# Performance work log

Measured on AMD Instinct MI355X. Metric: run time of the kernel, lower is better.

## Reference

```python
import jax, jax.numpy as jnp
import numpy as np

N_NODES = 100000
N_EDGES = 1600000
IN_CH = 128
HID = 64
OUT_CH = 10
N_GRAPHS = 64
NEG_SLOPE = 0.2   # GATv2Conv default negative_slope
EPS = 1e-16       # PyG softmax eps


def setup_inputs() -> dict:
    key = jax.random.key(0)
    ks = jax.random.split(key, 10)
    x = jax.random.normal(ks[0], (N_NODES, IN_CH), dtype=jnp.float32)
    edge_index = jax.random.randint(ks[1], (2, N_EDGES), 0, N_NODES, dtype=jnp.int64)
    batch = jnp.sort(jax.random.randint(ks[2], (N_NODES,), 0, N_GRAPHS, dtype=jnp.int64))
    s = 1.0 / np.sqrt(IN_CH)
    Wl = jax.random.uniform(ks[3], (IN_CH, HID), jnp.float32, -s, s)   # lin_l (source)
    Wr = jax.random.uniform(ks[4], (IN_CH, HID), jnp.float32, -s, s)   # lin_r (target)
    att = jax.random.uniform(ks[5], (HID,), jnp.float32, -1.0 / np.sqrt(HID), 1.0 / np.sqrt(HID))
    bias = jnp.zeros((HID,), jnp.float32)
    sf = 1.0 / np.sqrt(HID)
    fc_w = jax.random.uniform(ks[6], (HID, OUT_CH), jnp.float32, -sf, sf)
    fc_b = jax.random.uniform(ks[7], (OUT_CH,), jnp.float32, -sf, sf)
    return {"x": x, "Wl": Wl, "Wr": Wr, "att": att, "bias": bias,
            "fc_w": fc_w, "fc_b": fc_b, "edge_index": edge_index, "batch": batch}


def reference(x, Wl, Wr, att, bias, fc_w, fc_b, edge_index, batch):
    src, tgt = edge_index[0], edge_index[1]
    # GATv2Conv, heads=1: separate linear for source/target
    xl = x @ Wl                         # [N, H] messages (source side)
    xr = x @ Wr                         # [N, H] target side
    z = xl[src] + xr[tgt]               # [E, H]
    e = jnp.where(z > 0, z, NEG_SLOPE * z) @ att   # [E]
    # segment softmax over incoming edges of each target node
    m = jax.ops.segment_max(e, tgt, num_segments=N_NODES)      # [N]
    a = jnp.exp(e - m[tgt])                                    # [E]
    denom = jax.ops.segment_sum(a, tgt, num_segments=N_NODES)  # [N]
    alpha = a / (denom[tgt] + EPS)                             # [E]
    out = jax.ops.segment_sum(alpha[:, None] * xl[src], tgt, num_segments=N_NODES)
    out = out + bias                                           # [N, H]
    # global mean pool over graphs
    cnt = jax.ops.segment_sum(jnp.ones((N_NODES,), out.dtype), batch, num_segments=N_GRAPHS)
    pooled = jax.ops.segment_sum(out, batch, num_segments=N_GRAPHS) / jnp.maximum(cnt, 1.0)[:, None]
    h = jnp.where(pooled > 0, pooled, 0.01 * pooled)           # F.leaky_relu default slope
    # dropout is identity in eval / p=0
    return h @ fc_w + fc_b                                     # [G, OUT_CH]
```

## Files before the change

### kernel.cpp

```cpp
#include <hip/hip_runtime.h>
#include <hip/hip_bf16.h>

#define NN 100000
#define EE 1600000
#define CIN 128
#define HID 64
#define NG 64
#define NOUT 10
#define BSZ 32
#define NB 3125
#define NBA 3136
#define CAP 768
#define NBC 196
#define CCAP 9216

typedef short s16x8 __attribute__((ext_vector_type(8)));
typedef float f32x4 __attribute__((ext_vector_type(4)));

__device__ __forceinline__ unsigned short f2b(float f) {
  unsigned int b = __float_as_uint(f);
  return (unsigned short)((b + 0x7FFFu + ((b >> 16) & 1u)) >> 16);
}
__device__ __forceinline__ float b2f_lo(unsigned int u) {
  return __uint_as_float(u << 16);
}
__device__ __forceinline__ float b2f_hi(unsigned int u) {
  return __uint_as_float(u & 0xFFFF0000u);
}

__global__ __launch_bounds__(256) void k_prep(const float* __restrict__ Wl,
                                              const float* __restrict__ Wr,
                                              unsigned short* __restrict__ Wt) {
  int flat = blockIdx.x * 2048 + threadIdx.x;
  for (int i = 0; i < 8; ++i, flat += 256) {
    int n = flat & 127, k = flat >> 7;
    float v = (n < 64) ? Wl[k * 64 + n] : Wr[k * 64 + (n - 64)];
    Wt[n * 128 + k] = f2b(v);
  }
}

__global__ __launch_bounds__(256) void k_gemm(
    const float* __restrict__ x, const unsigned short* __restrict__ Wt,
    unsigned short* __restrict__ xl, unsigned short* __restrict__ xr) {
  __shared__ unsigned short A[128 * 128];
  __shared__ unsigned short B[128 * 128];
  const int tid = threadIdx.x;
  const int lane = tid & 63;
  const int w = tid >> 6;
  const int nb = blockIdx.x * 128;

  {
    int u = tid;
#pragma unroll
    for (int i = 0; i < 8; ++i, u += 256) {
      int n = u >> 4, slot = u & 15;
      uint4 v = *(const uint4*)((const char*)Wt + u * 16);
      int addr = n * 256 + ((slot * 16) ^ ((n & 7) << 4));
      *(uint4*)((char*)B + addr) = v;
    }
  }
  {
    int f = tid;
#pragma unroll
    for (int i = 0; i < 16; ++i, f += 256) {
      int row = f >> 5, c4 = f & 31;
      int node = nb + row;
      float4 v = make_float4(0.f, 0.f, 0.f, 0.f);
      if (node < NN) v = *(const float4*)(x + (long)node * CIN + c4 * 4);
      uint2 p;
      p.x = (unsigned)f2b(v.x) | ((unsigned)f2b(v.y) << 16);
      p.y = (unsigned)f2b(v.z) | ((unsigned)f2b(v.w) << 16);
      int base16 = row * 256 + (((c4 >> 1) << 4) ^ ((row & 7) << 4));
      *(uint2*)((char*)A + base16 + (c4 & 1) * 8) = p;
    }
  }
  __syncthreads();

  const int m0 = w * 32;
  f32x4 acc[2][8];
#pragma unroll
  for (int mt = 0; mt < 2; ++mt)
#pragma unroll
    for (int nt = 0; nt < 8; ++nt) acc[mt][nt] = (f32x4){0.f, 0.f, 0.f, 0.f};

#pragma unroll
  for (int ks = 0; ks < 4; ++ks) {
    const int kb2 = (ks * 32 + (lane >> 4) * 8) * 2;
    const int r0 = m0 + (lane & 15);
    const int r1 = r0 + 16;
    s16x8 a0 = *(const s16x8*)((char*)A + r0 * 256 + (kb2 ^ ((r0 & 7) << 4)));
    s16x8 a1 = *(const s16x8*)((char*)A + r1 * 256 + (kb2 ^ ((r1 & 7) << 4)));
#pragma unroll
    for (int nt = 0; nt < 8; ++nt) {
      const int col = nt * 16 + (lane & 15);
      s16x8 b =
          *(const s16x8*)((char*)B + col * 256 + (kb2 ^ ((col & 7) << 4)));
      acc[0][nt] =
          __builtin_amdgcn_mfma_f32_16x16x32_bf16(a0, b, acc[0][nt], 0, 0, 0);
      acc[1][nt] =
          __builtin_amdgcn_mfma_f32_16x16x32_bf16(a1, b, acc[1][nt], 0, 0, 0);
    }
  }
  __syncthreads();

#pragma unroll
  for (int mt = 0; mt < 2; ++mt) {
    const int rowb = m0 + mt * 16 + (lane >> 4) * 4;
#pragma unroll
    for (int nt = 0; nt < 8; ++nt) {
      const int col = nt * 16 + (lane & 15);
#pragma unroll
      for (int r = 0; r < 4; ++r)
        *((unsigned short*)A + (rowb + r) * 128 + col) = f2b(acc[mt][nt][r]);
    }
  }
  __syncthreads();

  {
    int u = tid;
#pragma unroll
    for (int i = 0; i < 8; ++i, u += 256) {
      int row = u >> 4, slot = u & 15;
      int node = nb + row;
      if (node < NN) {
        uint4 v = *(const uint4*)((const char*)A + row * 256 + slot * 16);
        if (slot < 8)
          *(uint4*)((char*)xl + (long)node * 128 + slot * 16) = v;
        else
          *(uint4*)((char*)xr + (long)node * 128 + (slot - 8) * 16) = v;
      }
    }
  }
}

__global__ __launch_bounds__(256) void k_coarse(const int* __restrict__ ei,
                                                int* __restrict__ gcurc,
                                                unsigned int* __restrict__ coarse) {
  __shared__ int hist[NBC], lbase[NBC], cur[NBC];
  const int tid = threadIdx.x;
  const int base = blockIdx.x * 4096;
  int ss[16], tt[16];
  for (int b = tid; b < NBC; b += 256) hist[b] = 0;
#pragma unroll
  for (int i = 0; i < 16; ++i) {
    int j = base + i * 256 + tid;
    if (j < EE) {
      ss[i] = ei[j];
      tt[i] = ei[EE + j];
    } else {
      tt[i] = -1;
    }
  }
  __syncthreads();
#pragma unroll
  for (int i = 0; i < 16; ++i)
    if (tt[i] >= 0) atomicAdd(&hist[tt[i] >> 9], 1);
  __syncthreads();
  for (int b = tid; b < NBC; b += 256) {
    int c = hist[b];
    lbase[b] = c ? atomicAdd(gcurc + b, c) : 0;
    cur[b] = 0;
  }
  __syncthreads();
#pragma unroll
  for (int i = 0; i < 16; ++i) {
    if (tt[i] >= 0) {
      int cb = tt[i] >> 9;
      int p = lbase[cb] + atomicAdd(&cur[cb], 1);
      if (p < CCAP)
        coarse[(long)cb * CCAP + p] =
            ((unsigned)ss[i] << 9) | (unsigned)(tt[i] & 511);
    }
  }
}

__global__ __launch_bounds__(256) void k_fine(
    const int* __restrict__ gcurc, const unsigned int* __restrict__ coarse,
    unsigned int* __restrict__ buckets, unsigned short* __restrict__ sc16,
    int* __restrict__ gcnt) {
  __shared__ unsigned int staged[CCAP];
  __shared__ int hist[512], sc[512], cur[512];
  __shared__ int ex32[16], csum[4], coffs[4];
  const int tid = threadIdx.x;
  const int c = blockIdx.x;
  const int ecnt = min(gcurc[c], CCAP);

  for (int i = tid; i < 512; i += 256) hist[i] = 0;
  __syncthreads();
  for (int i = tid; i < ecnt; i += 256) {
    unsigned v = coarse[(long)c * CCAP + i];
    staged[i] = v;
    atomicAdd(&hist[v & 511u], 1);
  }
  __syncthreads();

  {
    const int w = tid >> 6, lane = tid & 63;
    const int iA = w * 128 + lane, iB = iA + 64;
    int sA = hist[iA], sB = hist[iB];
#pragma unroll
    for (int off = 1; off < 64; off <<= 1) {
      int t1 = __shfl_up(sA, off, 64);
      int t2 = __shfl_up(sB, off, 64);
      if (lane >= off) { sA += t1; sB += t2; }
    }
    int tA = __shfl(sA, 63, 64);
    int tB = __shfl(sB, 63, 64);
    sc[iA] = sA;
    sc[iB] = sB + tA;
    if (lane == 0) csum[w] = tA + tB;
    __syncthreads();
    if (tid == 0) {
      int r = 0;
#pragma unroll
      for (int q = 0; q < 4; ++q) { coffs[q] = r; r += csum[q]; }
    }
    __syncthreads();
    sc[iA] += coffs[w];
    sc[iB] += coffs[w];
  }
  __syncthreads();

  if (tid < 16) ex32[tid] = sc[tid * 32] - hist[tid * 32];
  __syncthreads();
  for (int i = tid; i < 512; i += 256) {
    int f = i >> 5;
    int ex = sc[i] - hist[i];
    cur[i] = ex;
    int rel = ex - ex32[f];
    if (rel > CAP) rel = CAP;
    sc16[((long)c * 16 + f) * 32 + (i & 31)] = (unsigned short)rel;
  }
  if (tid < 16) {
    int fb = sc[tid * 32 + 31] - ex32[tid];
    gcnt[c * 16 + tid] = fb > CAP ? CAP : fb;
  }
  __syncthreads();
  for (int i = tid; i < ecnt; i += 256) {
    unsigned v = staged[i];
    int t9 = v & 511u;
    int p = atomicAdd(&cur[t9], 1);
    int rel = p - ex32[t9 >> 5];
    if (rel < CAP)
      buckets[((long)c * 16 + (t9 >> 5)) * CAP + rel] = v >> 9;
  }
}

__global__ __launch_bounds__(256) void k_pull2(
    const int* __restrict__ gcnt, const unsigned int* __restrict__ buckets,
    const unsigned short* __restrict__ sc16,
    const unsigned short* __restrict__ xl,
    const unsigned short* __restrict__ xr, const float* __restrict__ att,
    const float* __restrict__ bias, const int* __restrict__ batch,
    float* __restrict__ pooled, float* __restrict__ cnt) {
  __shared__ float pool2[2][HID];
  __shared__ float cnt2[2];
  const int tid = threadIdx.x;
  const int b = blockIdx.x;
  const int t0 = b << 5;
  if (tid < 2 * HID) ((float*)pool2)[tid] = 0.f;
  if (tid < 2) cnt2[tid] = 0.f;
  __syncthreads();

  const int l8 = tid & 7;
  const int d = tid >> 3;
  const int n = t0 + d;
  float av[8];
  {
    float4 alo = *(const float4*)(att + l8 * 8);
    float4 ahi = *(const float4*)(att + l8 * 8 + 4);
    av[0] = alo.x; av[1] = alo.y; av[2] = alo.z; av[3] = alo.w;
    av[4] = ahi.x; av[5] = ahi.y; av[6] = ahi.z; av[7] = ahi.w;
  }
  float xt[8];
  {
    uint4 ur = *(const uint4*)(xr + (long)n * HID + l8 * 8);
    xt[0] = b2f_lo(ur.x); xt[1] = b2f_hi(ur.x);
    xt[2] = b2f_lo(ur.y); xt[3] = b2f_hi(ur.y);
    xt[4] = b2f_lo(ur.z); xt[5] = b2f_hi(ur.z);
    xt[6] = b2f_lo(ur.w); xt[7] = b2f_hi(ur.w);
  }
  float acc[8] = {0.f, 0.f, 0.f, 0.f, 0.f, 0.f, 0.f, 0.f};
  float den = 0.f;
  const int e0 = sc16[(long)b * 32 + d];
  const int e1 = (d < 31) ? (int)sc16[(long)b * 32 + d + 1] : gcnt[b];
  const unsigned int* brow = buckets + (long)b * CAP;
  int e = e0;
  for (; e + 1 < e1; e += 2) {
    const int s0 = brow[e];
    const int s1 = brow[e + 1];
    const uint4 u0 = *(const uint4*)(xl + (long)s0 * HID + l8 * 8);
    const uint4 u1 = *(const uint4*)(xl + (long)s1 * HID + l8 * 8);
    float x0[8], x1[8];
    x0[0] = b2f_lo(u0.x); x0[1] = b2f_hi(u0.x);
    x0[2] = b2f_lo(u0.y); x0[3] = b2f_hi(u0.y);
    x0[4] = b2f_lo(u0.z); x0[5] = b2f_hi(u0.z);
    x0[6] = b2f_lo(u0.w); x0[7] = b2f_hi(u0.w);
    x1[0] = b2f_lo(u1.x); x1[1] = b2f_hi(u1.x);
    x1[2] = b2f_lo(u1.y); x1[3] = b2f_hi(u1.y);
    x1[4] = b2f_lo(u1.z); x1[5] = b2f_hi(u1.z);
    x1[6] = b2f_lo(u1.w); x1[7] = b2f_hi(u1.w);
    float p0 = 0.f, p1 = 0.f;
#pragma unroll
    for (int c = 0; c < 8; ++c) {
      float z0 = x0[c] + xt[c];
      float z1 = x1[c] + xt[c];
      z0 = z0 > 0.f ? z0 : 0.2f * z0;
      z1 = z1 > 0.f ? z1 : 0.2f * z1;
      p0 = fmaf(z0, av[c], p0);
      p1 = fmaf(z1, av[c], p1);
    }
    p0 += __shfl_xor(p0, 1, 8);
    p1 += __shfl_xor(p1, 1, 8);
    p0 += __shfl_xor(p0, 2, 8);
    p1 += __shfl_xor(p1, 2, 8);
    p0 += __shfl_xor(p0, 4, 8);
    p1 += __shfl_xor(p1, 4, 8);
    const float a0 = __expf(p0);
    const float a1 = __expf(p1);
    den += a0 + a1;
#pragma unroll
    for (int c = 0; c < 8; ++c) {
      acc[c] = fmaf(a0, x0[c], acc[c]);
      acc[c] = fmaf(a1, x1[c], acc[c]);
    }
  }
  if (e < e1) {
    const int s0 = brow[e];
    const uint4 u0 = *(const uint4*)(xl + (long)s0 * HID + l8 * 8);
    float x0[8];
    x0[0] = b2f_lo(u0.x); x0[1] = b2f_hi(u0.x);
    x0[2] = b2f_lo(u0.y); x0[3] = b2f_hi(u0.y);
    x0[4] = b2f_lo(u0.z); x0[5] = b2f_hi(u0.z);
    x0[6] = b2f_lo(u0.w); x0[7] = b2f_hi(u0.w);
    float p0 = 0.f;
#pragma unroll
    for (int c = 0; c < 8; ++c) {
      float z0 = x0[c] + xt[c];
      z0 = z0 > 0.f ? z0 : 0.2f * z0;
      p0 = fmaf(z0, av[c], p0);
    }
    p0 += __shfl_xor(p0, 1, 8);
    p0 += __shfl_xor(p0, 2, 8);
    p0 += __shfl_xor(p0, 4, 8);
    const float a0 = __expf(p0);
    den += a0;
#pragma unroll
    for (int c = 0; c < 8; ++c) acc[c] = fmaf(a0, x0[c], acc[c]);
  }
  const float inv = 1.f / (den + 1e-16f);
  const int gr = batch[n];
  const int idx = gr - batch[t0];
  float bv[8];
  {
    float4 blo = *(const float4*)(bias + l8 * 8);
    float4 bhi = *(const float4*)(bias + l8 * 8 + 4);
    bv[0] = blo.x; bv[1] = blo.y; bv[2] = blo.z; bv[3] = blo.w;
    bv[4] = bhi.x; bv[5] = bhi.y; bv[6] = bhi.z; bv[7] = bhi.w;
  }
  if (idx >= 0 && idx < 2) {
#pragma unroll
    for (int c = 0; c < 8; ++c)
      atomicAdd(&pool2[idx][l8 * 8 + c], fmaf(acc[c], inv, bv[c]));
    if (l8 == 0) atomicAdd(&cnt2[idx], 1.f);
  } else {
#pragma unroll
    for (int c = 0; c < 8; ++c)
      atomicAdd(pooled + gr * HID + l8 * 8 + c, fmaf(acc[c], inv, bv[c]));
    if (l8 == 0) atomicAdd(cnt + gr, 1.f);
  }
  __syncthreads();
  const int g0 = batch[t0];
  if (tid < 2 * HID) {
    const int which = tid >> 6, c = tid & 63;
    const int gg = g0 + which;
    const float val = pool2[which][c];
    if (gg < NG && val != 0.f) atomicAdd(pooled + gg * HID + c, val);
  }
  if (tid < 2) {
    const int gg = g0 + tid;
    if (gg < NG && cnt2[tid] != 0.f) atomicAdd(cnt + gg, cnt2[tid]);
  }
}

__global__ void k_final(const float* __restrict__ pooled,
                        const float* __restrict__ cnt,
                        const float* __restrict__ fc_w,
                        const float* __restrict__ fc_b,
                        float* __restrict__ out) {
  const int tid = threadIdx.x;
  if (tid >= NG * NOUT) return;
  const int gr = tid / NOUT, o = tid % NOUT;
  const float cg = fmaxf(cnt[gr], 1.0f);
  float acc = fc_b[o];
#pragma unroll 8
  for (int h = 0; h < HID; ++h) {
    float pv = pooled[gr * HID + h] / cg;
    float hv = pv > 0.f ? pv : 0.01f * pv;
    acc = fmaf(hv, fc_w[h * NOUT + o], acc);
  }
  out[gr * NOUT + o] = acc;
}

extern "C" void kernel_launch(void* const* d_in, const int* in_sizes, int n_in,
                              void* d_out, int out_size, void* d_ws,
                              size_t ws_size, hipStream_t stream) {
  const float* x = (const float*)d_in[0];
  const float* Wl = (const float*)d_in[1];
  const float* Wr = (const float*)d_in[2];
  const float* att = (const float*)d_in[3];
  const float* bias = (const float*)d_in[4];
  const float* fc_w = (const float*)d_in[5];
  const float* fc_b = (const float*)d_in[6];
  const int* ei = (const int*)d_in[7];
  const int* batch = (const int*)d_in[8];
  float* out = (float*)d_out;

  char* w = (char*)d_ws;
  unsigned short* xl = (unsigned short*)w;            w += (long)NN * HID * 2;
  unsigned short* xr = (unsigned short*)w;            w += (long)NN * HID * 2;
  unsigned short* Wt = (unsigned short*)w;            w += 128 * 128 * 2;
  unsigned int* coarse = (unsigned int*)w;            w += (long)NBC * CCAP * 4;
  unsigned int* buckets = (unsigned int*)w;           w += (long)NBA * CAP * 4;
  unsigned short* sc16 = (unsigned short*)w;          w += (long)NBA * 32 * 2;
  int* gcnt = (int*)w;                                w += NBA * 4;
  int* gcurc = (int*)w;                               w += NBC * 4;
  float* pooled = (float*)w;                          w += NG * HID * 4;
  float* cnt = (float*)w;                             w += NG * 4;

  hipMemsetAsync(gcurc, 0, (size_t)(NBC + NG * HID + NG) * sizeof(int),
                 stream);

  k_prep<<<8, 256, 0, stream>>>(Wl, Wr, Wt);
  k_gemm<<<(NN + 127) / 128, 256, 0, stream>>>(x, Wt, xl, xr);
  k_coarse<<<(EE + 4095) / 4096, 256, 0, stream>>>(ei, gcurc, coarse);
  k_fine<<<NBC, 256, 0, stream>>>(gcurc, coarse, buckets, sc16, gcnt);
  k_pull2<<<NB, 256, 0, stream>>>(gcnt, buckets, sc16, xl, xr, att, bias,
                                  batch, pooled, cnt);
  k_final<<<1, NG * NOUT, 0, stream>>>(pooled, cnt, fc_w, fc_b, out);
}
```

Before: 239.5 us.

## Switch CSR binning to 128-node coarse buckets, shrink GEMM and pull tiles

Edge bucketing now uses 782 coarse buckets of 128 target nodes, each with a single contiguous bucket array, instead of 196 buckets of 512 that were split into capped 32-node sub-buckets. The fine pass gets a simpler 128-entry scan. The GEMM tile drops to 64 rows and the pull kernel to 128 threads covering 16 nodes, which raises block count and occupancy. The zeroing memset is folded into k_prep, and the attention dot products use split accumulators to shorten dependency chains. Capacity per bucket is now 2432 edges, so overflow depends on degree skew.

```diff
diff --git a/kernel.cpp b/kernel.cpp
--- a/kernel.cpp
+++ b/kernel.cpp
@@ -7,12 +7,10 @@
 #define HID 64
 #define NG 64
 #define NOUT 10
-#define BSZ 32
-#define NB 3125
-#define NBA 3136
-#define CAP 768
-#define NBC 196
-#define CCAP 9216
+#define NBC2 782
+#define CCAP2 2432
+#define NPB 6250
+#define ZTOT (NBC2 + NG * HID + NG)
 
 typedef short s16x8 __attribute__((ext_vector_type(8)));
 typedef float f32x4 __attribute__((ext_vector_type(4)));
@@ -30,24 +28,28 @@
 
 __global__ __launch_bounds__(256) void k_prep(const float* __restrict__ Wl,
                                               const float* __restrict__ Wr,
-                                              unsigned short* __restrict__ Wt) {
+                                              unsigned short* __restrict__ Wt,
+                                              int* __restrict__ zbuf) {
   int flat = blockIdx.x * 2048 + threadIdx.x;
+#pragma unroll
   for (int i = 0; i < 8; ++i, flat += 256) {
     int n = flat & 127, k = flat >> 7;
     float v = (n < 64) ? Wl[k * 64 + n] : Wr[k * 64 + (n - 64)];
     Wt[n * 128 + k] = f2b(v);
   }
+  for (int z = blockIdx.x * 256 + threadIdx.x; z < ZTOT; z += 2048)
+    zbuf[z] = 0;
 }
 
 __global__ __launch_bounds__(256) void k_gemm(
     const float* __restrict__ x, const unsigned short* __restrict__ Wt,
     unsigned short* __restrict__ xl, unsigned short* __restrict__ xr) {
-  __shared__ unsigned short A[128 * 128];
+  __shared__ unsigned short A[64 * 128];
   __shared__ unsigned short B[128 * 128];
   const int tid = threadIdx.x;
   const int lane = tid & 63;
   const int w = tid >> 6;
-  const int nb = blockIdx.x * 128;
+  const int nb = blockIdx.x * 64;
 
   {
     int u = tid;
@@ -62,7 +64,7 @@
   {
     int f = tid;
 #pragma unroll
-    for (int i = 0; i < 16; ++i, f += 256) {
+    for (int i = 0; i < 8; ++i, f += 256) {
       int row = f >> 5, c4 = f & 31;
       int node = nb + row;
       float4 v = make_float4(0.f, 0.f, 0.f, 0.f);
@@ -76,42 +78,35 @@
   }
   __syncthreads();
 
-  const int m0 = w * 32;
-  f32x4 acc[2][8];
-#pragma unroll
-  for (int mt = 0; mt < 2; ++mt)
-#pragma unroll
-    for (int nt = 0; nt < 8; ++nt) acc[mt][nt] = (f32x4){0.f, 0.f, 0.f, 0.f};
+  const int m0 = w * 16;
+  f32x4 acc[8];
+#pragma unroll
+  for (int nt = 0; nt < 8; ++nt) acc[nt] = (f32x4){0.f, 0.f, 0.f, 0.f};
 
 #pragma unroll
   for (int ks = 0; ks < 4; ++ks) {
     const int kb2 = (ks * 32 + (lane >> 4) * 8) * 2;
     const int r0 = m0 + (lane & 15);
-    const int r1 = r0 + 16;
     s16x8 a0 = *(const s16x8*)((char*)A + r0 * 256 + (kb2 ^ ((r0 & 7) << 4)));
-    s16x8 a1 = *(const s16x8*)((char*)A + r1 * 256 + (kb2 ^ ((r1 & 7) << 4)));
 #pragma unroll
     for (int nt = 0; nt < 8; ++nt) {
       const int col = nt * 16 + (lane & 15);
       s16x8 b =
           *(const s16x8*)((char*)B + col * 256 + (kb2 ^ ((col & 7) << 4)));
-      acc[0][nt] =
-          __builtin_amdgcn_mfma_f32_16x16x32_bf16(a0, b, acc[0][nt], 0, 0, 0);
-      acc[1][nt] =
-          __builtin_amdgcn_mfma_f32_16x16x32_bf16(a1, b, acc[1][nt], 0, 0, 0);
-    }
-  }
-  __syncthreads();
-
-#pragma unroll
-  for (int mt = 0; mt < 2; ++mt) {
-    const int rowb = m0 + mt * 16 + (lane >> 4) * 4;
+      acc[nt] =
+          __builtin_amdgcn_mfma_f32_16x16x32_bf16(a0, b, acc[nt], 0, 0, 0);
+    }
+  }
+  __syncthreads();
+
+  {
+    const int rowb = m0 + (lane >> 4) * 4;
 #pragma unroll
     for (int nt = 0; nt < 8; ++nt) {
       const int col = nt * 16 + (lane & 15);
 #pragma unroll
       for (int r = 0; r < 4; ++r)
-        *((unsigned short*)A + (rowb + r) * 128 + col) = f2b(acc[mt][nt][r]);
+        *((unsigned short*)A + (rowb + r) * 128 + col) = f2b(acc[nt][r]);
     }
   }
   __syncthreads();
@@ -119,7 +114,7 @@
   {
     int u = tid;
 #pragma unroll
-    for (int i = 0; i < 8; ++i, u += 256) {
+    for (int i = 0; i < 4; ++i, u += 256) {
       int row = u >> 4, slot = u & 15;
       int node = nb + row;
       if (node < NN) {
@@ -136,11 +131,11 @@
 __global__ __launch_bounds__(256) void k_coarse(const int* __restrict__ ei,
                                                 int* __restrict__ gcurc,
                                                 unsigned int* __restrict__ coarse) {
-  __shared__ int hist[NBC], lbase[NBC], cur[NBC];
+  __shared__ int hist[NBC2], lbase[NBC2], cur[NBC2];
   const int tid = threadIdx.x;
   const int base = blockIdx.x * 4096;
   int ss[16], tt[16];
-  for (int b = tid; b < NBC; b += 256) hist[b] = 0;
+  for (int b = tid; b < NBC2; b += 256) hist[b] = 0;
 #pragma unroll
   for (int i = 0; i < 16; ++i) {
     int j = base + i * 256 + tid;
@@ -154,9 +149,9 @@
   __syncthreads();
 #pragma unroll
   for (int i = 0; i < 16; ++i)
-    if (tt[i] >= 0) atomicAdd(&hist[tt[i] >> 9], 1);
-  __syncthreads();
-  for (int b = tid; b < NBC; b += 256) {
+    if (tt[i] >= 0) atomicAdd(&hist[tt[i] >> 7], 1);
+  __syncthreads();
+  for (int b = tid; b < NBC2; b += 256) {
     int c = hist[b];
     lbase[b] = c ? atomicAdd(gcurc + b, c) : 0;
     cur[b] = 0;
@@ -165,11 +160,11 @@
 #pragma unroll
   for (int i = 0; i < 16; ++i) {
     if (tt[i] >= 0) {
-      int cb = tt[i] >> 9;
+      int cb = tt[i] >> 7;
       int p = lbase[cb] + atomicAdd(&cur[cb], 1);
-      if (p < CCAP)
-        coarse[(long)cb * CCAP + p] =
-            ((unsigned)ss[i] << 9) | (unsigned)(tt[i] & 511);
+      if (p < CCAP2)
+        coarse[(long)cb * CCAP2 + p] =
+            ((unsigned)ss[i] << 7) | (unsigned)(tt[i] & 127);
     }
   }
 }
@@ -178,75 +173,49 @@
     const int* __restrict__ gcurc, const unsigned int* __restrict__ coarse,
     unsigned int* __restrict__ buckets, unsigned short* __restrict__ sc16,
     int* __restrict__ gcnt) {
-  __shared__ unsigned int staged[CCAP];
-  __shared__ int hist[512], sc[512], cur[512];
-  __shared__ int ex32[16], csum[4], coffs[4];
+  __shared__ unsigned int staged[CCAP2];
+  __shared__ int hist[128], sc[128], cur[128];
   const int tid = threadIdx.x;
-  const int c = blockIdx.x;
-  const int ecnt = min(gcurc[c], CCAP);
-
-  for (int i = tid; i < 512; i += 256) hist[i] = 0;
+  const int cb = blockIdx.x;
+  const int ecnt = min(gcurc[cb], CCAP2);
+
+  if (tid < 128) hist[tid] = 0;
   __syncthreads();
   for (int i = tid; i < ecnt; i += 256) {
-    unsigned v = coarse[(long)c * CCAP + i];
+    unsigned v = coarse[(long)cb * CCAP2 + i];
     staged[i] = v;
-    atomicAdd(&hist[v & 511u], 1);
-  }
-  __syncthreads();
-
-  {
-    const int w = tid >> 6, lane = tid & 63;
-    const int iA = w * 128 + lane, iB = iA + 64;
-    int sA = hist[iA], sB = hist[iB];
+    atomicAdd(&hist[v & 127u], 1);
+  }
+  __syncthreads();
+
+  if (tid < 128) {
+    const int lane = tid & 63;
+    int v = hist[tid], sum = v;
 #pragma unroll
     for (int off = 1; off < 64; off <<= 1) {
-      int t1 = __shfl_up(sA, off, 64);
-      int t2 = __shfl_up(sB, off, 64);
-      if (lane >= off) { sA += t1; sB += t2; }
-    }
-    int tA = __shfl(sA, 63, 64);
-    int tB = __shfl(sB, 63, 64);
-    sc[iA] = sA;
-    sc[iB] = sB + tA;
-    if (lane == 0) csum[w] = tA + tB;
-    __syncthreads();
-    if (tid == 0) {
-      int r = 0;
-#pragma unroll
-      for (int q = 0; q < 4; ++q) { coffs[q] = r; r += csum[q]; }
-    }
-    __syncthreads();
-    sc[iA] += coffs[w];
-    sc[iB] += coffs[w];
-  }
-  __syncthreads();
-
-  if (tid < 16) ex32[tid] = sc[tid * 32] - hist[tid * 32];
-  __syncthreads();
-  for (int i = tid; i < 512; i += 256) {
-    int f = i >> 5;
-    int ex = sc[i] - hist[i];
-    cur[i] = ex;
-    int rel = ex - ex32[f];
-    if (rel > CAP) rel = CAP;
-    sc16[((long)c * 16 + f) * 32 + (i & 31)] = (unsigned short)rel;
-  }
-  if (tid < 16) {
-    int fb = sc[tid * 32 + 31] - ex32[tid];
-    gcnt[c * 16 + tid] = fb > CAP ? CAP : fb;
-  }
+      int t = __shfl_up(sum, off, 64);
+      if (lane >= off) sum += t;
+    }
+    sc[tid] = sum;
+  }
+  __syncthreads();
+  if (tid >= 64 && tid < 128) sc[tid] += sc[63];
+  __syncthreads();
+  if (tid < 128) {
+    int st = sc[tid] - hist[tid];
+    cur[tid] = st;
+    sc16[(long)cb * 128 + tid] = (unsigned short)st;
+  }
+  if (tid == 0) gcnt[cb] = ecnt;
   __syncthreads();
   for (int i = tid; i < ecnt; i += 256) {
     unsigned v = staged[i];
-    int t9 = v & 511u;
-    int p = atomicAdd(&cur[t9], 1);
-    int rel = p - ex32[t9 >> 5];
-    if (rel < CAP)
-      buckets[((long)c * 16 + (t9 >> 5)) * CAP + rel] = v >> 9;
-  }
-}
-
-__global__ __launch_bounds__(256) void k_pull2(
+    int p = atomicAdd(&cur[v & 127u], 1);
+    buckets[(long)cb * CCAP2 + p] = v >> 7;
+  }
+}
+
+__global__ __launch_bounds__(128) void k_pull2(
     const int* __restrict__ gcnt, const unsigned int* __restrict__ buckets,
     const unsigned short* __restrict__ sc16,
     const unsigned short* __restrict__ xl,
@@ -256,15 +225,16 @@
   __shared__ float pool2[2][HID];
   __shared__ float cnt2[2];
   const int tid = threadIdx.x;
-  const int b = blockIdx.x;
-  const int t0 = b << 5;
-  if (tid < 2 * HID) ((float*)pool2)[tid] = 0.f;
+  const int n0 = blockIdx.x * 16;
+  pool2[tid >> 6][tid & 63] = 0.f;
   if (tid < 2) cnt2[tid] = 0.f;
   __syncthreads();
 
   const int l8 = tid & 7;
   const int d = tid >> 3;
-  const int n = t0 + d;
+  const int n = n0 + d;
+  const int cb = n >> 7;
+  const int tl = n & 127;
   float av[8];
   {
     float4 alo = *(const float4*)(att + l8 * 8);
@@ -282,9 +252,9 @@
   }
   float acc[8] = {0.f, 0.f, 0.f, 0.f, 0.f, 0.f, 0.f, 0.f};
   float den = 0.f;
-  const int e0 = sc16[(long)b * 32 + d];
-  const int e1 = (d < 31) ? (int)sc16[(long)b * 32 + d + 1] : gcnt[b];
-  const unsigned int* brow = buckets + (long)b * CAP;
+  const int e0 = sc16[(long)cb * 128 + tl];
+  const int e1 = (tl < 127) ? (int)sc16[(long)cb * 128 + tl + 1] : gcnt[cb];
+  const unsigned int* brow = buckets + (long)cb * CCAP2;
   int e = e0;
   for (; e + 1 < e1; e += 2) {
     const int s0 = brow[e];
@@ -300,16 +270,24 @@
     x1[2] = b2f_lo(u1.y); x1[3] = b2f_hi(u1.y);
     x1[4] = b2f_lo(u1.z); x1[5] = b2f_hi(u1.z);
     x1[6] = b2f_lo(u1.w); x1[7] = b2f_hi(u1.w);
-    float p0 = 0.f, p1 = 0.f;
-#pragma unroll
-    for (int c = 0; c < 8; ++c) {
-      float z0 = x0[c] + xt[c];
-      float z1 = x1[c] + xt[c];
-      z0 = z0 > 0.f ? z0 : 0.2f * z0;
-      z1 = z1 > 0.f ? z1 : 0.2f * z1;
-      p0 = fmaf(z0, av[c], p0);
-      p1 = fmaf(z1, av[c], p1);
-    }
+    float p0a = 0.f, p0b = 0.f, p1a = 0.f, p1b = 0.f;
+#pragma unroll
+    for (int c = 0; c < 8; c += 2) {
+      float za = x0[c] + xt[c];
+      float zb = x0[c + 1] + xt[c + 1];
+      za = za > 0.f ? za : 0.2f * za;
+      zb = zb > 0.f ? zb : 0.2f * zb;
+      p0a = fmaf(za, av[c], p0a);
+      p0b = fmaf(zb, av[c + 1], p0b);
+      float wa = x1[c] + xt[c];
+      float wb = x1[c + 1] + xt[c + 1];
+      wa = wa > 0.f ? wa : 0.2f * wa;
+      wb = wb > 0.f ? wb : 0.2f * wb;
+      p1a = fmaf(wa, av[c], p1a);
+      p1b = fmaf(wb, av[c + 1], p1b);
+    }
+    float p0 = p0a + p0b;
+    float p1 = p1a + p1b;
     p0 += __shfl_xor(p0, 1, 8);
     p1 += __shfl_xor(p1, 1, 8);
     p0 += __shfl_xor(p0, 2, 8);
@@ -333,13 +311,17 @@
     x0[2] = b2f_lo(u0.y); x0[3] = b2f_hi(u0.y);
     x0[4] = b2f_lo(u0.z); x0[5] = b2f_hi(u0.z);
     x0[6] = b2f_lo(u0.w); x0[7] = b2f_hi(u0.w);
-    float p0 = 0.f;
-#pragma unroll
-    for (int c = 0; c < 8; ++c) {
-      float z0 = x0[c] + xt[c];
-      z0 = z0 > 0.f ? z0 : 0.2f * z0;
-      p0 = fmaf(z0, av[c], p0);
-    }
+    float pa = 0.f, pb = 0.f;
+#pragma unroll
+    for (int c = 0; c < 8; c += 2) {
+      float za = x0[c] + xt[c];
+      float zb = x0[c + 1] + xt[c + 1];
+      za = za > 0.f ? za : 0.2f * za;
+      zb = zb > 0.f ? zb : 0.2f * zb;
+      pa = fmaf(za, av[c], pa);
+      pb = fmaf(zb, av[c + 1], pb);
+    }
+    float p0 = pa + pb;
     p0 += __shfl_xor(p0, 1, 8);
     p0 += __shfl_xor(p0, 2, 8);
     p0 += __shfl_xor(p0, 4, 8);
@@ -350,7 +332,8 @@
   }
   const float inv = 1.f / (den + 1e-16f);
   const int gr = batch[n];
-  const int idx = gr - batch[t0];
+  const int g0 = batch[n0];
+  const int idx = gr - g0;
   float bv[8];
   {
     float4 blo = *(const float4*)(bias + l8 * 8);
@@ -370,8 +353,7 @@
     if (l8 == 0) atomicAdd(cnt + gr, 1.f);
   }
   __syncthreads();
-  const int g0 = batch[t0];
-  if (tid < 2 * HID) {
+  {
     const int which = tid >> 6, c = tid & 63;
     const int gg = g0 + which;
     const float val = pool2[which][c];
@@ -417,25 +399,22 @@
   float* out = (float*)d_out;
 
   char* w = (char*)d_ws;
-  unsigned short* xl = (unsigned short*)w;            w += (long)NN * HID * 2;
-  unsigned short* xr = (unsigned short*)w;            w += (long)NN * HID * 2;
-  unsigned short* Wt = (unsigned short*)w;            w += 128 * 128 * 2;
-  unsigned int* coarse = (unsigned int*)w;            w += (long)NBC * CCAP * 4;
-  unsigned int* buckets = (unsigned int*)w;           w += (long)NBA * CAP * 4;
-  unsigned short* sc16 = (unsigned short*)w;          w += (long)NBA * 32 * 2;
-  int* gcnt = (int*)w;                                w += NBA * 4;
-  int* gcurc = (int*)w;                               w += NBC * 4;
-  float* pooled = (float*)w;                          w += NG * HID * 4;
-  float* cnt = (float*)w;                             w += NG * 4;
-
-  hipMemsetAsync(gcurc, 0, (size_t)(NBC + NG * HID + NG) * sizeof(int),
-                 stream);
-
-  k_prep<<<8, 256, 0, stream>>>(Wl, Wr, Wt);
-  k_gemm<<<(NN + 127) / 128, 256, 0, stream>>>(x, Wt, xl, xr);
+  unsigned short* xl = (unsigned short*)w;      w += (long)NN * HID * 2;
+  unsigned short* xr = (unsigned short*)w;      w += (long)NN * HID * 2;
+  unsigned short* Wt = (unsigned short*)w;      w += 128 * 128 * 2;
+  unsigned int* coarse = (unsigned int*)w;      w += (long)NBC2 * CCAP2 * 4;
+  unsigned int* buckets = (unsigned int*)w;     w += (long)NBC2 * CCAP2 * 4;
+  unsigned short* sc16 = (unsigned short*)w;    w += (long)NBC2 * 128 * 2;
+  int* gcnt = (int*)w;                          w += NBC2 * 4;
+  int* gcurc = (int*)w;                         w += NBC2 * 4;
+  float* pooled = (float*)w;                    w += NG * HID * 4;
+  float* cnt = (float*)w;                       w += NG * 4;
+
+  k_prep<<<8, 256, 0, stream>>>(Wl, Wr, Wt, gcurc);
+  k_gemm<<<(NN + 63) / 64, 256, 0, stream>>>(x, Wt, xl, xr);
   k_coarse<<<(EE + 4095) / 4096, 256, 0, stream>>>(ei, gcurc, coarse);
-  k_fine<<<NBC, 256, 0, stream>>>(gcurc, coarse, buckets, sc16, gcnt);
-  k_pull2<<<NB, 256, 0, stream>>>(gcnt, buckets, sc16, xl, xr, att, bias,
-                                  batch, pooled, cnt);
+  k_fine<<<NBC2, 256, 0, stream>>>(gcurc, coarse, buckets, sc16, gcnt);
+  k_pull2<<<NPB, 128, 0, stream>>>(gcnt, buckets, sc16, xl, xr, att, bias,
+                                   batch, pooled, cnt);
   k_final<<<1, NG * NOUT, 0, stream>>>(pooled, cnt, fc_w, fc_b, out);
 }
```

Result: slower. 248.8 us (+3.9%).
